# Optimization experiments

Hardware: AMD Instinct MI355X
Metric: run time of the kernel (lower is better)

## Reference

```python
import jax, jax.numpy as jnp
import numpy as np

N_NODES = 100000
NEG_SLOPE = 0.2  # PyG GATConv default negative_slope


def gat_layer(x, src, dst, W, a_src, a_dst, b):
    """PyG-style GATConv (eval mode: dropout = identity), concat=True.
    x: [N, F_in]; W: [F_in, H*C]; a_src/a_dst: [H, C]; b: [H*C].
    src/dst: [E] edge endpoints (messages flow src -> dst), self-loops included.
    """
    N = x.shape[0]
    H, C = a_src.shape
    h = (x @ W).reshape(N, H, C)                       # [N, H, C]
    al_s = jnp.sum(h * a_src, axis=-1)                 # [N, H]
    al_d = jnp.sum(h * a_dst, axis=-1)                 # [N, H]
    e = jax.nn.leaky_relu(al_s[src] + al_d[dst], NEG_SLOPE)  # [E, H]
    # softmax over incoming edges of each dst node (every node has a self-loop)
    m = jax.ops.segment_max(e, dst, num_segments=N)    # [N, H]
    ex = jnp.exp(e - m[dst])
    s = jax.ops.segment_sum(ex, dst, num_segments=N)   # [N, H]
    alpha = ex / s[dst]                                # [E, H]
    out = jax.ops.segment_sum(h[src] * alpha[:, :, None], dst, num_segments=N)
    return out.reshape(N, H * C) + b


def setup_inputs() -> dict:
    key = jax.random.key(0)
    ks = jax.random.split(key, 12)
    F_in, Hc, H, n_cls = 128, 32, 4, 3
    x = jax.random.normal(ks[0], (N_NODES, F_in), dtype=jnp.float32)
    edge_index = jax.random.randint(ks[1], (2, 1600000), 0, N_NODES, dtype=jnp.int64)
    sc1 = 1.0 / np.sqrt(F_in)
    sc2 = 1.0 / np.sqrt(Hc * H)
    return {
        "x": x,
        "edge_index": edge_index,
        "W1": jax.random.normal(ks[2], (F_in, H * Hc), dtype=jnp.float32) * sc1,
        "a1_src": jax.random.normal(ks[3], (H, Hc), dtype=jnp.float32) * sc1,
        "a1_dst": jax.random.normal(ks[4], (H, Hc), dtype=jnp.float32) * sc1,
        "b1": jnp.zeros((H * Hc,), dtype=jnp.float32),
        "W2": jax.random.normal(ks[5], (H * Hc, Hc), dtype=jnp.float32) * sc2,
        "a2_src": jax.random.normal(ks[6], (1, Hc), dtype=jnp.float32) * sc2,
        "a2_dst": jax.random.normal(ks[7], (1, Hc), dtype=jnp.float32) * sc2,
        "b2": jnp.zeros((Hc,), dtype=jnp.float32),
        "lin_W": jax.random.normal(ks[8], (Hc, n_cls), dtype=jnp.float32) * (1.0 / np.sqrt(Hc)),
        "lin_b": jnp.zeros((n_cls,), dtype=jnp.float32),
    }


def reference(x, edge_index, W1, a1_src, a1_dst, b1, W2, a2_src, a2_dst, b2, lin_W, lin_b):
    N = x.shape[0]
    loops = jnp.arange(N, dtype=edge_index.dtype)
    src = jnp.concatenate([edge_index[0], loops])
    dst = jnp.concatenate([edge_index[1], loops])
    h = jax.nn.elu(gat_layer(x, src, dst, W1, a1_src, a1_dst, b1))
    h = gat_layer(h, src, dst, W2, a2_src, a2_dst, b2)
    pooled = h.mean(axis=0, keepdims=True)             # batch=None path: [1, Hc]
    return jax.nn.softmax(pooled @ lin_W + lin_b, axis=1)
```

## Files before the change

kernel.cpp:

```cpp
#include <hip/hip_runtime.h>
#include <cstdint>
#include <cstddef>

static inline size_t align_up(size_t v, size_t a) { return (v + a - 1) & ~(a - 1); }

#define BCAP 3072

typedef __attribute__((ext_vector_type(8))) short short8;
typedef __attribute__((ext_vector_type(4))) float f32x4;
typedef __attribute__((ext_vector_type(2))) float f32x2;

__device__ inline unsigned short bf16_1(float x) {
  unsigned u = __float_as_uint(x);
  u += 0x7FFFu + ((u >> 16) & 1u);
  return (unsigned short)(u >> 16);
}
__device__ inline unsigned bfpack(float x, float y) {
  unsigned ux = __float_as_uint(x); ux += 0x7FFFu + ((ux >> 16) & 1u);
  unsigned uy = __float_as_uint(y); uy += 0x7FFFu + ((uy >> 16) & 1u);
  return (ux >> 16) | (uy & 0xFFFF0000u);
}

__device__ inline unsigned char fp8_1(float x) {
  return (unsigned char)(__builtin_amdgcn_cvt_pk_fp8_f32(x, x, 0, false) & 0xFF);
}

__global__ void detect_kernel(const unsigned int* e, int n_check, int* flag) {
  __shared__ int bad;
  if (threadIdx.x == 0) bad = 0;
  __syncthreads();
  for (int i = threadIdx.x; i < n_check; i += blockDim.x)
    if (e[2 * i + 1] != 0u) bad = 1;
  __syncthreads();
  if (threadIdx.x == 0) *flag = bad ? 0 : 1;
}

__device__ inline int load_edge(const void* eidx, int is64, size_t idx) {
  if (is64) return (int)((const long long*)eidx)[idx];
  return ((const int*)eidx)[idx];
}

__global__ void prep_kernel(const float* __restrict__ W1, const float* __restrict__ W2,
                            unsigned short* __restrict__ w1t, unsigned short* __restrict__ w2t) {
  int t = blockIdx.x * 256 + threadIdx.x;
  if (t < 16384) {
    int c = t >> 7, k = t & 127;
    w1t[t] = bf16_1(W1[(size_t)k * 128 + c]);
  } else if (t < 20480) {
    int i = t - 16384;
    int c = i >> 7, k = i & 127;
    w2t[i] = bf16_1(W2[(size_t)k * 32 + c]);
  }
}


__global__ __launch_bounds__(256) void sortA_kernel(const void* eidx, const int* flag, int E,
                                                    int* __restrict__ fillB,
                                                    unsigned* __restrict__ packed, int NB) {
  __shared__ int hist[1024];
  __shared__ int loff[1024];
  __shared__ int lbase[1024];
  __shared__ int lcnt[1024];
  __shared__ unsigned sortedV[2048];
  __shared__ unsigned short sortedB[2048];
  const int t = threadIdx.x;
  const int chunk0 = blockIdx.x * 2048;
  const int cntE = min(2048, E - chunk0);
  const int is64 = *flag;
  int sv[8], dv[8];
  for (int i = t; i < 1024; i += 256) { hist[i] = 0; lcnt[i] = 0; }
  __syncthreads();
#pragma unroll
  for (int it = 0; it < 8; ++it) {
    int li = it * 256 + t;
    if (li < cntE) {
      sv[it] = load_edge(eidx, is64, (size_t)chunk0 + li);
      dv[it] = load_edge(eidx, is64, (size_t)E + chunk0 + li);
      atomicAdd(&hist[dv[it] >> 7], 1);
    }
  }
  __syncthreads();
  for (int b = t; b < NB; b += 256) {
    int h = hist[b];
    if (h) lbase[b] = b * BCAP + atomicAdd(&fillB[b], h);
  }
  {
    int base = t * 4;
    int v[4]; int s = 0;
    __shared__ int sd[256];
#pragma unroll
    for (int j = 0; j < 4; ++j) { v[j] = hist[base + j]; s += v[j]; }
    sd[t] = s; __syncthreads();
    for (int off = 1; off < 256; off <<= 1) {
      int u = (t >= off) ? sd[t - off] : 0;
      __syncthreads();
      sd[t] += u;
      __syncthreads();
    }
    int run = sd[t] - s;
#pragma unroll
    for (int j = 0; j < 4; ++j) { loff[base + j] = run; run += v[j]; }
  }
  __syncthreads();
#pragma unroll
  for (int it = 0; it < 8; ++it) {
    int li = it * 256 + t;
    if (li < cntE) {
      int b = dv[it] >> 7;
      int r = atomicAdd(&lcnt[b], 1);
      int pos = loff[b] + r;
      sortedV[pos] = (unsigned)sv[it] | ((unsigned)(dv[it] & 127) << 20);
      sortedB[pos] = (unsigned short)b;
    }
  }
  __syncthreads();
  for (int li = t; li < cntE; li += 256) {
    int b = sortedB[li];
    packed[(size_t)lbase[b] + (li - loff[b])] = sortedV[li];
  }
}

__global__ __launch_bounds__(256) void buildCSR_kernel(const unsigned* __restrict__ packed,
                                                       const int* __restrict__ fillB,
                                                       int* __restrict__ rowbeg,
                                                       int* __restrict__ rowend,
                                                       int* __restrict__ csr, int N, int NB) {
  __shared__ int cnt[128], ex[128], fill[128];
  const int b = blockIdx.x;
  const int t = threadIdx.x;
  const int beg = b * BCAP;
  const int end = beg + fillB[b];
  const int node0 = b << 7;
  const int nn = min(128, N - node0);
  if (t < 128) { cnt[t] = 0; fill[t] = 0; }
  __syncthreads();
  for (int i = beg + t; i < end; i += 256) {
    int j = (packed[i] >> 20) & 127;
    atomicAdd(&cnt[j], 1);
  }
  __syncthreads();
  if (t < 128) ex[t] = cnt[t];
  __syncthreads();
  for (int off = 1; off < 128; off <<= 1) {
    int u = (t >= off && t < 128) ? ex[t - off] : 0;
    __syncthreads();
    if (t < 128) ex[t] += u;
    __syncthreads();
  }
  if (t < 128) ex[t] -= cnt[t];
  __syncthreads();
  if (t < nn) {
    rowbeg[node0 + t] = beg + ex[t];
    rowend[node0 + t] = beg + ex[t] + cnt[t];
  }
  for (int i = beg + t; i < end; i += 256) {
    unsigned v = packed[i];
    int j = (v >> 20) & 127;
    int r = atomicAdd(&fill[j], 1);
    csr[beg + ex[j] + r] = (int)(v & 0xFFFFFu);
  }
}

__global__ __launch_bounds__(256) void gemm1_mfma(
    const float* __restrict__ x, const unsigned short* __restrict__ w1t,
    const float* __restrict__ a1s, const float* __restrict__ a1d,
    unsigned char* __restrict__ h1f, float* __restrict__ al1s, float* __restrict__ al1d, int N) {
  __shared__ unsigned short sw[128 * 136];
  __shared__ unsigned short sx[64 * 136];
  unsigned char* ftile = (unsigned char*)sx;
  const int t = threadIdx.x;
  const int row0 = blockIdx.x * 64;
  for (int i = t; i < 4096; i += 256) {
    int c = i >> 5, k4 = (i & 31) * 4;
    *(ushort4*)&sw[c * 136 + k4] = *(const ushort4*)&w1t[c * 128 + k4];
  }
  for (int i = t; i < 2048; i += 256) {
    int r = i >> 5, c4 = (i & 31) * 4;
    float4 v = make_float4(0.f, 0.f, 0.f, 0.f);
    if (row0 + r < N) v = *(const float4*)(x + (size_t)(row0 + r) * 128 + c4);
    ushort4 b; b.x = bf16_1(v.x); b.y = bf16_1(v.y); b.z = bf16_1(v.z); b.w = bf16_1(v.w);
    *(ushort4*)&sx[r * 136 + c4] = b;
  }
  __syncthreads();
  const int lane = t & 63, wave = t >> 6;
  const int m = lane & 15, quad = lane >> 4;
  const unsigned short* arow = &sx[(wave * 16 + m) * 136];
  short8 A[4];
#pragma unroll
  for (int ks = 0; ks < 4; ++ks) A[ks] = *(const short8*)&arow[ks * 32 + quad * 8];
  __syncthreads();
  const int lrow = wave * 16 + quad * 4;
#pragma unroll
  for (int nt = 0; nt < 8; ++nt) {
    const unsigned short* brow = &sw[(nt * 16 + m) * 136];
    f32x4 acc = {0.f, 0.f, 0.f, 0.f};
#pragma unroll
    for (int ks = 0; ks < 4; ++ks) {
      short8 B = *(const short8*)&brow[ks * 32 + quad * 8];
      acc = __builtin_amdgcn_mfma_f32_16x16x32_bf16(A[ks], B, acc, 0, 0, 0);
    }
#pragma unroll
    for (int r = 0; r < 4; ++r)
      ftile[(lrow + r) * 128 + nt * 16 + m] = fp8_1(acc[r]);
  }
  __syncthreads();
#pragma unroll
  for (int it = 0; it < 2; ++it) {
    int row = it * 32 + (t >> 3);
    int chunk = t & 7;
    uint4 v = *(const uint4*)&ftile[row * 128 + chunk * 16];
    int grow = row0 + row;
    if (grow < N) *(uint4*)&h1f[(size_t)grow * 128 + chunk * 16] = v;
    unsigned w[4] = {v.x, v.y, v.z, v.w};
    float ps = 0.f, pd = 0.f;
    int cb = chunk * 16;
#pragma unroll
    for (int q = 0; q < 4; ++q) {
      f32x2 lo = __builtin_amdgcn_cvt_pk_f32_fp8((int)w[q], false);
      f32x2 hi = __builtin_amdgcn_cvt_pk_f32_fp8((int)w[q], true);
      int c = cb + q * 4;
      ps += lo[0] * a1s[c] + lo[1] * a1s[c + 1] + hi[0] * a1s[c + 2] + hi[1] * a1s[c + 3];
      pd += lo[0] * a1d[c] + lo[1] * a1d[c + 1] + hi[0] * a1d[c + 2] + hi[1] * a1d[c + 3];
    }
    ps += __shfl_xor(ps, 1); pd += __shfl_xor(pd, 1);
    if ((chunk & 1) == 0 && grow < N) {
      int head = chunk >> 1;
      al1s[(size_t)grow * 4 + head] = ps;
      al1d[(size_t)grow * 4 + head] = pd;
    }
  }
}

__global__ __launch_bounds__(256) void gemm2_mfma(
    const unsigned* __restrict__ houtb, const unsigned short* __restrict__ w2t,
    const float* __restrict__ a2s, const float* __restrict__ a2d,
    unsigned char* __restrict__ h2f, float* __restrict__ al2s, float* __restrict__ al2d, int N) {
  __shared__ unsigned short sw[32 * 136];
  __shared__ unsigned short sx[64 * 136];
  unsigned char* ftile = (unsigned char*)sx;
  const int t = threadIdx.x;
  const int row0 = blockIdx.x * 64;
  for (int i = t; i < 1024; i += 256) {
    int c = i >> 5, k4 = (i & 31) * 4;
    *(ushort4*)&sw[c * 136 + k4] = *(const ushort4*)&w2t[c * 128 + k4];
  }
  for (int i = t; i < 2048; i += 256) {
    int r = i >> 5, d2 = (i & 31) * 2;
    uint2 v = make_uint2(0u, 0u);
    if (row0 + r < N) v = *(const uint2*)(houtb + (size_t)(row0 + r) * 64 + d2);
    *(uint2*)&sx[r * 136 + d2 * 2] = v;
  }
  __syncthreads();
  const int lane = t & 63, wave = t >> 6;
  const int m = lane & 15, quad = lane >> 4;
  const unsigned short* arow = &sx[(wave * 16 + m) * 136];
  short8 A[4];
#pragma unroll
  for (int ks = 0; ks < 4; ++ks) A[ks] = *(const short8*)&arow[ks * 32 + quad * 8];
  __syncthreads();
  const int lrow = wave * 16 + quad * 4;
#pragma unroll
  for (int nt = 0; nt < 2; ++nt) {
    const unsigned short* brow = &sw[(nt * 16 + m) * 136];
    f32x4 acc = {0.f, 0.f, 0.f, 0.f};
#pragma unroll
    for (int ks = 0; ks < 4; ++ks) {
      short8 B = *(const short8*)&brow[ks * 32 + quad * 8];
      acc = __builtin_amdgcn_mfma_f32_16x16x32_bf16(A[ks], B, acc, 0, 0, 0);
    }
#pragma unroll
    for (int r = 0; r < 4; ++r)
      ftile[(lrow + r) * 32 + nt * 16 + m] = fp8_1(acc[r]);
  }
  __syncthreads();
  if (t < 128) {
    int row = t >> 1, chunk = t & 1;
    uint4 v = *(const uint4*)&ftile[row * 32 + chunk * 16];
    int grow = row0 + row;
    if (grow < N) *(uint4*)&h2f[(size_t)grow * 32 + chunk * 16] = v;
    unsigned w[4] = {v.x, v.y, v.z, v.w};
    float ps = 0.f, pd = 0.f;
    int cb = chunk * 16;
#pragma unroll
    for (int q = 0; q < 4; ++q) {
      f32x2 lo = __builtin_amdgcn_cvt_pk_f32_fp8((int)w[q], false);
      f32x2 hi = __builtin_amdgcn_cvt_pk_f32_fp8((int)w[q], true);
      int c = cb + q * 4;
      ps += lo[0] * a2s[c] + lo[1] * a2s[c + 1] + hi[0] * a2s[c + 2] + hi[1] * a2s[c + 3];
      pd += lo[0] * a2d[c] + lo[1] * a2d[c + 1] + hi[0] * a2d[c + 2] + hi[1] * a2d[c + 3];
    }
    ps += __shfl_xor(ps, 1); pd += __shfl_xor(pd, 1);
    if (chunk == 0 && grow < N) { al2s[grow] = ps; al2d[grow] = pd; }
  }
}

#define DEC8P(HV, EX)                                                       \
  {                                                                         \
    f32x2 _e2; _e2[0] = (EX); _e2[1] = (EX);                                \
    acc01 += __builtin_amdgcn_cvt_pk_f32_fp8((int)(HV).x, false) * _e2;     \
    acc23 += __builtin_amdgcn_cvt_pk_f32_fp8((int)(HV).x, true) * _e2;      \
    acc45 += __builtin_amdgcn_cvt_pk_f32_fp8((int)(HV).y, false) * _e2;     \
    acc67 += __builtin_amdgcn_cvt_pk_f32_fp8((int)(HV).y, true) * _e2;      \
    den += (EX);                                                            \
  }

__global__ __launch_bounds__(256) void agg1_kernel(
    const int* __restrict__ rowbeg, const int* __restrict__ rowend, const int* __restrict__ csr_src,
    const unsigned char* __restrict__ h1f,
    const float* __restrict__ al_s, const float* __restrict__ al_d,
    const float* __restrict__ b1, unsigned* __restrict__ houtb, int N) {
  int t = threadIdx.x;
  int d = (blockIdx.x * 256 + t) >> 6;
  if (d >= N) return;
  int lane = t & 63;
  int e_id = lane >> 4;
  unsigned c8 = (unsigned)(lane & 15);
  unsigned head = c8 >> 2;
  const unsigned boff = c8 * 8u;
  const float ald = al_d[(unsigned)d * 4u + head];
  f32x2 acc01 = {0.f, 0.f}, acc23 = {0.f, 0.f}, acc45 = {0.f, 0.f}, acc67 = {0.f, 0.f};
  float den = 0.f;
  {
    float e = al_s[(unsigned)d * 4u + head] + ald;
    e = fmaxf(e, 0.2f * e);
    float ex = (e_id == 0) ? __expf(e) : 0.f;
    uint2 hv = *(const uint2*)(h1f + (((unsigned)d << 7) | boff));
    DEC8P(hv, ex);
  }
  const int beg = __builtin_amdgcn_readfirstlane(rowbeg[d]);
  const int end = __builtin_amdgcn_readfirstlane(rowend[d]);
  for (int i = beg; i < end; i += 8) {
    int idx0 = i + e_id;
    int idx1 = idx0 + 4;
    int sj0 = (idx0 < end) ? csr_src[(unsigned)idx0] : d;
    int sj1 = (idx1 < end) ? csr_src[(unsigned)idx1] : d;
    float as0 = al_s[(unsigned)sj0 * 4u + head];
    float as1 = al_s[(unsigned)sj1 * 4u + head];
    uint2 hv0 = *(const uint2*)(h1f + (((unsigned)sj0 << 7) | boff));
    uint2 hv1 = *(const uint2*)(h1f + (((unsigned)sj1 << 7) | boff));
    float e0 = as0 + ald;
    e0 = fmaxf(e0, 0.2f * e0);
    float ex0 = __expf(e0);
    if (idx0 >= end) ex0 = 0.f;
    float e1 = as1 + ald;
    e1 = fmaxf(e1, 0.2f * e1);
    float ex1 = __expf(e1);
    if (idx1 >= end) ex1 = 0.f;
    DEC8P(hv0, ex0);
    DEC8P(hv1, ex1);
  }
  float a0 = acc01[0], a1 = acc01[1], a2 = acc23[0], a3 = acc23[1];
  float a4 = acc45[0], a5 = acc45[1], a6 = acc67[0], a7 = acc67[1];
  a0 += __shfl_xor(a0, 16); a1 += __shfl_xor(a1, 16);
  a2 += __shfl_xor(a2, 16); a3 += __shfl_xor(a3, 16);
  a4 += __shfl_xor(a4, 16); a5 += __shfl_xor(a5, 16);
  a6 += __shfl_xor(a6, 16); a7 += __shfl_xor(a7, 16);
  den += __shfl_xor(den, 16);
  a0 += __shfl_xor(a0, 32); a1 += __shfl_xor(a1, 32);
  a2 += __shfl_xor(a2, 32); a3 += __shfl_xor(a3, 32);
  a4 += __shfl_xor(a4, 32); a5 += __shfl_xor(a5, 32);
  a6 += __shfl_xor(a6, 32); a7 += __shfl_xor(a7, 32);
  den += __shfl_xor(den, 32);
  float inv = 1.f / den;
  float4 bv0 = *(const float4*)(b1 + 8 * c8);
  float4 bv1 = *(const float4*)(b1 + 8 * c8 + 4);
  float o0 = a0 * inv + bv0.x;
  float o1 = a1 * inv + bv0.y;
  float o2 = a2 * inv + bv0.z;
  float o3 = a3 * inv + bv0.w;
  float o4 = a4 * inv + bv1.x;
  float o5 = a5 * inv + bv1.y;
  float o6 = a6 * inv + bv1.z;
  float o7 = a7 * inv + bv1.w;
  o0 = o0 > 0.f ? o0 : __expf(o0) - 1.f;
  o1 = o1 > 0.f ? o1 : __expf(o1) - 1.f;
  o2 = o2 > 0.f ? o2 : __expf(o2) - 1.f;
  o3 = o3 > 0.f ? o3 : __expf(o3) - 1.f;
  o4 = o4 > 0.f ? o4 : __expf(o4) - 1.f;
  o5 = o5 > 0.f ? o5 : __expf(o5) - 1.f;
  o6 = o6 > 0.f ? o6 : __expf(o6) - 1.f;
  o7 = o7 > 0.f ? o7 : __expf(o7) - 1.f;
  if (e_id == 0) {
    uint4 u;
    u.x = bfpack(o0, o1); u.y = bfpack(o2, o3);
    u.z = bfpack(o4, o5); u.w = bfpack(o6, o7);
    *(uint4*)&houtb[(unsigned)d * 64u + 4u * c8] = u;
  }
}

__global__ __launch_bounds__(256) void agg2_kernel(
    const int* __restrict__ rowbeg, const int* __restrict__ rowend, const int* __restrict__ csr_src,
    const unsigned char* __restrict__ h2f,
    const float* __restrict__ al_s, const float* __restrict__ al_d,
    float* __restrict__ partial, int N) {
  __shared__ float sp[16 * 32];
  int t = threadIdx.x;
  int l16 = t & 15;
  int slot = t >> 4;
  int node = (blockIdx.x * 256 + t) >> 4;
  int e_id = l16 >> 2;
  unsigned c8 = (unsigned)(l16 & 3);
  const unsigned boff = c8 * 8u;
  float o0 = 0.f, o1 = 0.f, o2 = 0.f, o3 = 0.f;
  float o4 = 0.f, o5 = 0.f, o6 = 0.f, o7 = 0.f;
  if (node < N) {
    const float ald = al_d[node];
    f32x2 acc01 = {0.f, 0.f}, acc23 = {0.f, 0.f}, acc45 = {0.f, 0.f}, acc67 = {0.f, 0.f};
    float den = 0.f;
    {
      float e = al_s[node] + ald;
      e = fmaxf(e, 0.2f * e);
      float ex = (e_id == 0) ? __expf(e) : 0.f;
      uint2 hv = *(const uint2*)(h2f + (((unsigned)node << 5) | boff));
      DEC8P(hv, ex);
    }
    const int beg = rowbeg[node], end = rowend[node];
    for (int i = beg; i < end; i += 8) {
      int idx0 = i + e_id;
      int idx1 = idx0 + 4;
      int sj0 = (idx0 < end) ? csr_src[(unsigned)idx0] : node;
      int sj1 = (idx1 < end) ? csr_src[(unsigned)idx1] : node;
      float as0 = al_s[(unsigned)sj0];
      float as1 = al_s[(unsigned)sj1];
      uint2 hv0 = *(const uint2*)(h2f + (((unsigned)sj0 << 5) | boff));
      uint2 hv1 = *(const uint2*)(h2f + (((unsigned)sj1 << 5) | boff));
      float e0 = as0 + ald;
      e0 = fmaxf(e0, 0.2f * e0);
      float ex0 = __expf(e0);
      if (idx0 >= end) ex0 = 0.f;
      float e1 = as1 + ald;
      e1 = fmaxf(e1, 0.2f * e1);
      float ex1 = __expf(e1);
      if (idx1 >= end) ex1 = 0.f;
      DEC8P(hv0, ex0);
      DEC8P(hv1, ex1);
    }
    float a0 = acc01[0], a1 = acc01[1], a2 = acc23[0], a3 = acc23[1];
    float a4 = acc45[0], a5 = acc45[1], a6 = acc67[0], a7 = acc67[1];
    a0 += __shfl_xor(a0, 4); a1 += __shfl_xor(a1, 4);
    a2 += __shfl_xor(a2, 4); a3 += __shfl_xor(a3, 4);
    a4 += __shfl_xor(a4, 4); a5 += __shfl_xor(a5, 4);
    a6 += __shfl_xor(a6, 4); a7 += __shfl_xor(a7, 4);
    den += __shfl_xor(den, 4);
    a0 += __shfl_xor(a0, 8); a1 += __shfl_xor(a1, 8);
    a2 += __shfl_xor(a2, 8); a3 += __shfl_xor(a3, 8);
    a4 += __shfl_xor(a4, 8); a5 += __shfl_xor(a5, 8);
    a6 += __shfl_xor(a6, 8); a7 += __shfl_xor(a7, 8);
    den += __shfl_xor(den, 8);
    float inv = 1.f / den;
    o0 = a0 * inv; o1 = a1 * inv; o2 = a2 * inv; o3 = a3 * inv;
    o4 = a4 * inv; o5 = a5 * inv; o6 = a6 * inv; o7 = a7 * inv;
  }
  if (e_id == 0) {
    float4 v0 = {o0, o1, o2, o3};
    float4 v1 = {o4, o5, o6, o7};
    *(float4*)&sp[slot * 32 + 8 * c8] = v0;
    *(float4*)&sp[slot * 32 + 8 * c8 + 4] = v1;
  }
  __syncthreads();
  if (t < 32) {
    float s = 0.f;
#pragma unroll
    for (int j = 0; j < 16; ++j) s += sp[j * 32 + t];
    partial[(size_t)blockIdx.x * 32 + t] = s;
  }
}

__global__ __launch_bounds__(256) void reduce_kernel(
    const float* __restrict__ partial, int nb, float* __restrict__ partial2) {
  __shared__ float sp[8 * 32];
  int t = threadIdx.x;
  int slot = t >> 5, c = t & 31;
  int row0 = blockIdx.x * 8 + slot;
  float s = 0.f;
  for (int i = row0; i < nb; i += 1024) s += partial[(size_t)i * 32 + c];
  sp[slot * 32 + c] = s;
  __syncthreads();
  if (t < 32) {
    float tot = 0.f;
#pragma unroll
    for (int j = 0; j < 8; ++j) tot += sp[j * 32 + t];
    partial2[(size_t)blockIdx.x * 32 + t] = tot;
  }
}

__global__ void final_kernel(const float* __restrict__ partial2, int nb,
                             const float* __restrict__ b2, const float* __restrict__ linW,
                             const float* __restrict__ linb, float* __restrict__ out, int N) {
  __shared__ float sd[256];
  __shared__ float pooled[32];
  int t = threadIdx.x;
  int c = t & 31, g = t >> 5;
  float s = 0.f;
  for (int i = g; i < nb; i += 8) s += partial2[(size_t)i * 32 + c];
  sd[t] = s; __syncthreads();
  if (t < 32) {
    float tot = 0.f;
#pragma unroll
    for (int j = 0; j < 8; ++j) tot += sd[j * 32 + t];
    pooled[t] = tot / (float)N + b2[t];
  }
  __syncthreads();
  if (t == 0) {
    float lg[3];
    for (int j = 0; j < 3; ++j) lg[j] = linb[j];
    for (int cc = 0; cc < 32; ++cc)
      for (int j = 0; j < 3; ++j) lg[j] += pooled[cc] * linW[cc * 3 + j];
    float m = fmaxf(lg[0], fmaxf(lg[1], lg[2]));
    float e0 = __expf(lg[0] - m), e1 = __expf(lg[1] - m), e2 = __expf(lg[2] - m);
    float inv = 1.f / (e0 + e1 + e2);
    out[0] = e0 * inv; out[1] = e1 * inv; out[2] = e2 * inv;
  }
}

extern "C" void kernel_launch(void* const* d_in, const int* in_sizes, int n_in,
                              void* d_out, int out_size, void* d_ws, size_t ws_size,
                              hipStream_t stream) {
  const float* x    = (const float*)d_in[0];
  const void*  eidx = d_in[1];
  const float* W1   = (const float*)d_in[2];
  const float* a1s  = (const float*)d_in[3];
  const float* a1d  = (const float*)d_in[4];
  const float* b1   = (const float*)d_in[5];
  const float* W2   = (const float*)d_in[6];
  const float* a2s  = (const float*)d_in[7];
  const float* a2d  = (const float*)d_in[8];
  const float* b2   = (const float*)d_in[9];
  const float* linW = (const float*)d_in[10];
  const float* linb = (const float*)d_in[11];
  float* out = (float*)d_out;

  const int N = in_sizes[0] / 128;
  const int E = in_sizes[1] / 2;
  const int NB = (N + 127) >> 7;

  char* ws = (char*)d_ws;
  size_t off = 0;
  auto alloc = [&](size_t bytes) -> void* {
    size_t o = off;
    off = align_up(off + bytes, 256);
    return (void*)(ws + o);
  };
  int* fillB  = (int*)alloc((size_t)1024 * sizeof(int));
  int* flag   = (int*)alloc(sizeof(int));
  int* rowbeg = (int*)alloc((size_t)N * sizeof(int));
  int* rowend = (int*)alloc((size_t)N * sizeof(int));
  unsigned* packed = (unsigned*)alloc((size_t)NB * BCAP * sizeof(unsigned));
  int* csr    = (int*)alloc((size_t)NB * BCAP * sizeof(int));
  float* al1s = (float*)alloc((size_t)N * 4 * sizeof(float));
  float* al1d = (float*)alloc((size_t)N * 4 * sizeof(float));
  float* al2s = (float*)alloc((size_t)N * sizeof(float));
  float* al2d = (float*)alloc((size_t)N * sizeof(float));
  unsigned short* w1t = (unsigned short*)alloc(16384 * sizeof(unsigned short));
  unsigned short* w2t = (unsigned short*)alloc(4096 * sizeof(unsigned short));
  unsigned char* h1f  = (unsigned char*)alloc((size_t)N * 128);
  unsigned* houtb = (unsigned*)alloc((size_t)N * 64 * sizeof(unsigned));
  unsigned char* h2f  = (unsigned char*)alloc((size_t)N * 32);
  const int nAggBlocks = (N + 15) / 16;
  float* partial  = (float*)alloc((size_t)nAggBlocks * 32 * sizeof(float));
  float* partial2 = (float*)alloc((size_t)128 * 32 * sizeof(float));

  hipMemsetAsync(fillB, 0, (size_t)1024 * sizeof(int), stream);
  int ncheck = E < 512 ? E : 512;
  detect_kernel<<<1, 256, 0, stream>>>((const unsigned int*)eidx, ncheck, flag);
  prep_kernel<<<80, 256, 0, stream>>>(W1, W2, w1t, w2t);

  sortA_kernel<<<(E + 2047) / 2048, 256, 0, stream>>>(eidx, flag, E, fillB, packed, NB);
  buildCSR_kernel<<<NB, 256, 0, stream>>>(packed, fillB, rowbeg, rowend, csr, N, NB);

  const int gemmBlocks = (N + 63) / 64;
  gemm1_mfma<<<gemmBlocks, 256, 0, stream>>>(x, w1t, a1s, a1d, h1f, al1s, al1d, N);
  agg1_kernel<<<(N * 64 + 255) / 256, 256, 0, stream>>>(
      rowbeg, rowend, csr, h1f, al1s, al1d, b1, houtb, N);
  gemm2_mfma<<<gemmBlocks, 256, 0, stream>>>(houtb, w2t, a2s, a2d, h2f, al2s, al2d, N);
  agg2_kernel<<<(N * 16 + 255) / 256, 256, 0, stream>>>(
      rowbeg, rowend, csr, h2f, al2s, al2d, partial, N);
  reduce_kernel<<<128, 256, 0, stream>>>(partial, nAggBlocks, partial2);
  final_kernel<<<1, 256, 0, stream>>>(partial2, 128, b2, linW, linb, out, N);
}
```

Measured before the change: 284.7 us.

## Fold memset and dtype detection into kernels; software-prefetch CSR indices in aggregation

Drops the hipMemsetAsync and the separate detect kernel. fillB is now zeroed inside prep_kernel, and each sortA block decides on its own whether the edge indices are int64 by checking its own chunk. This removes two stream operations and their launch gaps. The agg1 and agg2 loops now fetch the next iteration's csr_src indices one step ahead, which shortens the dependent load chain at the cost of extra registers. The per-block detection is a heuristic that can misjudge a chunk that happens to have all-zero high words.

```diff
diff --git a/kernel.cpp b/kernel.cpp
--- a/kernel.cpp
+++ b/kernel.cpp
@@ -25,23 +25,9 @@
   return (unsigned char)(__builtin_amdgcn_cvt_pk_fp8_f32(x, x, 0, false) & 0xFF);
 }
 
-__global__ void detect_kernel(const unsigned int* e, int n_check, int* flag) {
-  __shared__ int bad;
-  if (threadIdx.x == 0) bad = 0;
-  __syncthreads();
-  for (int i = threadIdx.x; i < n_check; i += blockDim.x)
-    if (e[2 * i + 1] != 0u) bad = 1;
-  __syncthreads();
-  if (threadIdx.x == 0) *flag = bad ? 0 : 1;
-}
-
-__device__ inline int load_edge(const void* eidx, int is64, size_t idx) {
-  if (is64) return (int)((const long long*)eidx)[idx];
-  return ((const int*)eidx)[idx];
-}
-
 __global__ void prep_kernel(const float* __restrict__ W1, const float* __restrict__ W2,
-                            unsigned short* __restrict__ w1t, unsigned short* __restrict__ w2t) {
+                            unsigned short* __restrict__ w1t, unsigned short* __restrict__ w2t,
+                            int* __restrict__ fillB) {
   int t = blockIdx.x * 256 + threadIdx.x;
   if (t < 16384) {
     int c = t >> 7, k = t & 127;
@@ -50,11 +36,18 @@
     int i = t - 16384;
     int c = i >> 7, k = i & 127;
     w2t[i] = bf16_1(W2[(size_t)k * 32 + c]);
-  }
-}
-
-
-__global__ __launch_bounds__(256) void sortA_kernel(const void* eidx, const int* flag, int E,
+  } else if (t < 21504) {
+    fillB[t - 20480] = 0;
+  }
+}
+
+
+__device__ inline int load_edge(const void* eidx, int is64, size_t idx) {
+  if (is64) return (int)((const long long*)eidx)[idx];
+  return ((const int*)eidx)[idx];
+}
+
+__global__ __launch_bounds__(256) void sortA_kernel(const void* eidx, int E,
                                                     int* __restrict__ fillB,
                                                     unsigned* __restrict__ packed, int NB) {
   __shared__ int hist[1024];
@@ -63,13 +56,21 @@
   __shared__ int lcnt[1024];
   __shared__ unsigned sortedV[2048];
   __shared__ unsigned short sortedB[2048];
+  __shared__ int s_is64;
   const int t = threadIdx.x;
   const int chunk0 = blockIdx.x * 2048;
   const int cntE = min(2048, E - chunk0);
-  const int is64 = *flag;
+  if (t == 0) s_is64 = 1;
+  for (int i = t; i < 1024; i += 256) { hist[i] = 0; lcnt[i] = 0; }
+  __syncthreads();
+  {
+    int nchk = min(cntE, 256);
+    for (int i = t; i < nchk; i += 256)
+      if (((const unsigned*)eidx)[2 * (size_t)(chunk0 + i) + 1] != 0u) s_is64 = 0;
+  }
+  __syncthreads();
+  const int is64 = s_is64;
   int sv[8], dv[8];
-  for (int i = t; i < 1024; i += 256) { hist[i] = 0; lcnt[i] = 0; }
-  __syncthreads();
 #pragma unroll
   for (int it = 0; it < 8; ++it) {
     int li = it * 256 + t;
@@ -318,6 +319,12 @@
   unsigned head = c8 >> 2;
   const unsigned boff = c8 * 8u;
   const float ald = al_d[(unsigned)d * 4u + head];
+  const int beg = __builtin_amdgcn_readfirstlane(rowbeg[d]);
+  const int end = __builtin_amdgcn_readfirstlane(rowend[d]);
+  int idx0 = beg + e_id;
+  int idx1 = idx0 + 4;
+  int sj0 = (idx0 < end) ? csr_src[(unsigned)idx0] : d;
+  int sj1 = (idx1 < end) ? csr_src[(unsigned)idx1] : d;
   f32x2 acc01 = {0.f, 0.f}, acc23 = {0.f, 0.f}, acc45 = {0.f, 0.f}, acc67 = {0.f, 0.f};
   float den = 0.f;
   {
@@ -327,25 +334,24 @@
     uint2 hv = *(const uint2*)(h1f + (((unsigned)d << 7) | boff));
     DEC8P(hv, ex);
   }
-  const int beg = __builtin_amdgcn_readfirstlane(rowbeg[d]);
-  const int end = __builtin_amdgcn_readfirstlane(rowend[d]);
   for (int i = beg; i < end; i += 8) {
-    int idx0 = i + e_id;
-    int idx1 = idx0 + 4;
-    int sj0 = (idx0 < end) ? csr_src[(unsigned)idx0] : d;
-    int sj1 = (idx1 < end) ? csr_src[(unsigned)idx1] : d;
-    float as0 = al_s[(unsigned)sj0 * 4u + head];
-    float as1 = al_s[(unsigned)sj1 * 4u + head];
-    uint2 hv0 = *(const uint2*)(h1f + (((unsigned)sj0 << 7) | boff));
-    uint2 hv1 = *(const uint2*)(h1f + (((unsigned)sj1 << 7) | boff));
+    const int cidx0 = idx0, cidx1 = idx1;
+    const int csj0 = sj0, csj1 = sj1;
+    float as0 = al_s[(unsigned)csj0 * 4u + head];
+    float as1 = al_s[(unsigned)csj1 * 4u + head];
+    uint2 hv0 = *(const uint2*)(h1f + (((unsigned)csj0 << 7) | boff));
+    uint2 hv1 = *(const uint2*)(h1f + (((unsigned)csj1 << 7) | boff));
+    idx0 += 8; idx1 += 8;
+    sj0 = (idx0 < end) ? csr_src[(unsigned)idx0] : d;
+    sj1 = (idx1 < end) ? csr_src[(unsigned)idx1] : d;
     float e0 = as0 + ald;
     e0 = fmaxf(e0, 0.2f * e0);
     float ex0 = __expf(e0);
-    if (idx0 >= end) ex0 = 0.f;
+    if (cidx0 >= end) ex0 = 0.f;
     float e1 = as1 + ald;
     e1 = fmaxf(e1, 0.2f * e1);
     float ex1 = __expf(e1);
-    if (idx1 >= end) ex1 = 0.f;
+    if (cidx1 >= end) ex1 = 0.f;
     DEC8P(hv0, ex0);
     DEC8P(hv1, ex1);
   }
@@ -405,6 +411,11 @@
   float o4 = 0.f, o5 = 0.f, o6 = 0.f, o7 = 0.f;
   if (node < N) {
     const float ald = al_d[node];
+    const int beg = rowbeg[node], end = rowend[node];
+    int idx0 = beg + e_id;
+    int idx1 = idx0 + 4;
+    int sj0 = (idx0 < end) ? csr_src[(unsigned)idx0] : node;
+    int sj1 = (idx1 < end) ? csr_src[(unsigned)idx1] : node;
     f32x2 acc01 = {0.f, 0.f}, acc23 = {0.f, 0.f}, acc45 = {0.f, 0.f}, acc67 = {0.f, 0.f};
     float den = 0.f;
     {
@@ -414,24 +425,24 @@
       uint2 hv = *(const uint2*)(h2f + (((unsigned)node << 5) | boff));
       DEC8P(hv, ex);
     }
-    const int beg = rowbeg[node], end = rowend[node];
     for (int i = beg; i < end; i += 8) {
-      int idx0 = i + e_id;
-      int idx1 = idx0 + 4;
-      int sj0 = (idx0 < end) ? csr_src[(unsigned)idx0] : node;
-      int sj1 = (idx1 < end) ? csr_src[(unsigned)idx1] : node;
-      float as0 = al_s[(unsigned)sj0];
-      float as1 = al_s[(unsigned)sj1];
-      uint2 hv0 = *(const uint2*)(h2f + (((unsigned)sj0 << 5) | boff));
-      uint2 hv1 = *(const uint2*)(h2f + (((unsigned)sj1 << 5) | boff));
+      const int cidx0 = idx0, cidx1 = idx1;
+      const int csj0 = sj0, csj1 = sj1;
+      float as0 = al_s[(unsigned)csj0];
+      float as1 = al_s[(unsigned)csj1];
+      uint2 hv0 = *(const uint2*)(h2f + (((unsigned)csj0 << 5) | boff));
+      uint2 hv1 = *(const uint2*)(h2f + (((unsigned)csj1 << 5) | boff));
+      idx0 += 8; idx1 += 8;
+      sj0 = (idx0 < end) ? csr_src[(unsigned)idx0] : node;
+      sj1 = (idx1 < end) ? csr_src[(unsigned)idx1] : node;
       float e0 = as0 + ald;
       e0 = fmaxf(e0, 0.2f * e0);
       float ex0 = __expf(e0);
-      if (idx0 >= end) ex0 = 0.f;
+      if (cidx0 >= end) ex0 = 0.f;
       float e1 = as1 + ald;
       e1 = fmaxf(e1, 0.2f * e1);
       float ex1 = __expf(e1);
-      if (idx1 >= end) ex1 = 0.f;
+      if (cidx1 >= end) ex1 = 0.f;
       DEC8P(hv0, ex0);
       DEC8P(hv1, ex1);
     }
@@ -542,7 +553,6 @@
     return (void*)(ws + o);
   };
   int* fillB  = (int*)alloc((size_t)1024 * sizeof(int));
-  int* flag   = (int*)alloc(sizeof(int));
   int* rowbeg = (int*)alloc((size_t)N * sizeof(int));
   int* rowend = (int*)alloc((size_t)N * sizeof(int));
   unsigned* packed = (unsigned*)alloc((size_t)NB * BCAP * sizeof(unsigned));
@@ -560,12 +570,9 @@
   float* partial  = (float*)alloc((size_t)nAggBlocks * 32 * sizeof(float));
   float* partial2 = (float*)alloc((size_t)128 * 32 * sizeof(float));
 
-  hipMemsetAsync(fillB, 0, (size_t)1024 * sizeof(int), stream);
-  int ncheck = E < 512 ? E : 512;
-  detect_kernel<<<1, 256, 0, stream>>>((const unsigned int*)eidx, ncheck, flag);
-  prep_kernel<<<80, 256, 0, stream>>>(W1, W2, w1t, w2t);
-
-  sortA_kernel<<<(E + 2047) / 2048, 256, 0, stream>>>(eidx, flag, E, fillB, packed, NB);
+  prep_kernel<<<84, 256, 0, stream>>>(W1, W2, w1t, w2t, fillB);
+
+  sortA_kernel<<<(E + 2047) / 2048, 256, 0, stream>>>(eidx, E, fillB, packed, NB);
   buildCSR_kernel<<<NB, 256, 0, stream>>>(packed, fillB, rowbeg, rowend, csr, N, NB);
 
   const int gemmBlocks = (N + 63) / 64;
```

Result: faster. 270.3 us (-5.1%).
